# Kernel optimization log

Hardware: AMD Instinct MI355X
Metric: run time of the kernel (lower is better)

Reference implementation:

```python
import jax, jax.numpy as jnp
import numpy as np


def _rotate_half(x):
    a, b = jnp.split(x, 2, axis=-1)
    return jnp.concatenate([-b, a], axis=-1)


def _rope_tables(L, d, dtype):
    inv = 1.0 / (10000.0 ** (jnp.arange(0, d, 2, dtype=jnp.float32) / d))
    ang = jnp.arange(L, dtype=jnp.float32)[:, None] * inv[None, :]  # (L, d/2)
    cos = jnp.repeat(jnp.cos(ang), 2, axis=-1)[None, :, None, :].astype(dtype)  # (1,L,1,d)
    sin = jnp.repeat(jnp.sin(ang), 2, axis=-1)[None, :, None, :].astype(dtype)
    return cos, sin


def setup_inputs() -> dict:
    key = jax.random.key(0)
    ks = jax.random.split(key, 7)
    B, L, D, h = 1, 1024, 768, 12
    d = D // h
    s = 0.02
    return {
        "X": jax.random.normal(ks[0], (B, L, D), jnp.float32),
        "Wq": jax.random.normal(ks[1], (D, D), jnp.float32) * s,
        "Wk": jax.random.normal(ks[2], (D, D), jnp.float32) * s,
        "Wv": jax.random.normal(ks[3], (D, D), jnp.float32) * s,
        "Wu": jax.random.normal(ks[4], (D, D), jnp.float32) * s,
        "Wg": jax.random.normal(ks[5], (3 * h, D), jnp.float32) * s,
        "Wo": jax.random.normal(ks[6], (D, D), jnp.float32) * s,
        "prior_mu": jnp.zeros((1, 1, h, d), jnp.float32),
        "prior_log_tau": jnp.zeros((1, 1, h, 1), jnp.float32),
    }


def _forward(X, Wq, Wk, Wv, Wu, Wg, Wo, prior_mu, prior_log_tau):
    B, L, D = X.shape
    h = prior_mu.shape[2]
    d = D // h
    eps = 1e-12
    # projections (torch Linear: x @ W.T, no bias)
    q = (X @ Wq.T).reshape(B, L, h, d)
    k = (X @ Wk.T).reshape(B, L, h, d)
    v = (X @ Wv.T).reshape(B, L, h, d)
    u = (X @ Wu.T).reshape(B, L, h, d)
    gate = (X @ Wg.T).reshape(B, L, h, 3)
    t = jnp.arange(1, L + 1, dtype=X.dtype).reshape(1, L, 1, 1)
    # calculate_logit (logit_type='deviation', causal)
    log_tau = jnp.exp(jnp.clip(prior_log_tau, -50.0, 30.0))
    u_sum = jnp.cumsum(u, axis=1)
    bar_u = (log_tau * prior_mu + u_sum) / (log_tau + t)
    s_i = -jnp.sum(u * bar_u, axis=-1, keepdims=True) / np.float32(np.sqrt(d))  # (B,L,h,1)
    # RoPE + L2 normalize q, k
    cos, sin = _rope_tables(L, d, X.dtype)
    q = q * cos + _rotate_half(q) * sin
    k = k * cos + _rotate_half(k) * sin
    q = q / jnp.maximum(jnp.linalg.norm(q, axis=-1, keepdims=True), eps)
    k = k / jnp.maximum(jnp.linalg.norm(k, axis=-1, keepdims=True), eps)
    # associative causal branch of compute_o
    s_max = jax.lax.stop_gradient(jnp.max(s_i, axis=1, keepdims=True))
    exp_s = jnp.exp(s_i - s_max)              # (B,L,h,1)
    E_t = jnp.cumsum(exp_s, axis=1)
    P_t = jnp.cumsum(s_i, axis=1)
    kv = jnp.einsum('blhd,blhe->blhde', k, v)  # (B,L,h,d,d)
    F_t = jnp.cumsum(exp_s[..., None] * kv, axis=1)
    G_t = jnp.cumsum(s_i[..., None] * kv, axis=1)
    H_t = jnp.cumsum(kv, axis=1)
    sig1 = jax.nn.sigmoid(gate[..., 0:1])      # (B,L,h,1)
    sigh = jax.nn.sigmoid(gate[..., 1:2])
    alpha = sigh / (E_t + eps)
    beta = (sig1 - sigh) / t
    gamma = -((beta * P_t + sigh) / t)
    M = alpha[..., None] * F_t + beta[..., None] * G_t + gamma[..., None] * H_t
    out = jnp.einsum('blhd,blhde->blhe', q, M)  # (B,L,h,d)
    # LayerNorm over head dim, eps=1e-5, no affine
    mu = jnp.mean(out, axis=-1, keepdims=True)
    var = jnp.mean(jnp.square(out - mu), axis=-1, keepdims=True)
    out = (out - mu) / jnp.sqrt(var + 1e-5)
    # output projection (dropout=0.0 -> identity)
    return out.reshape(B, L, D) @ Wo.T


def reference(X, Wq, Wk, Wv, Wu, Wg, Wo, prior_mu, prior_log_tau):
    return _forward(X, Wq, Wk, Wv, Wu, Wg, Wo, prior_mu, prior_log_tau)
```

## Files before the change

### kernel.cpp

```cpp
#include <hip/hip_runtime.h>
#include <hip/hip_bf16.h>
#include <math.h>

typedef __attribute__((ext_vector_type(8))) short bf16x8;
typedef __attribute__((ext_vector_type(4))) float f32x4;

#define SEQ 1024
#define DIM 768
#define NH 12
#define HD 64


__device__ __forceinline__ float wave_reduce_sum(float v) {
    for (int off = 1; off < 64; off <<= 1) v += __shfl_xor(v, off);
    return v;
}
__device__ __forceinline__ short f2bs(float x) {
    __hip_bfloat16 h = __float2bfloat16(x);
    return *reinterpret_cast<short*>(&h);
}
__device__ __forceinline__ float bs2f(short x) {
    __hip_bfloat16 h = *reinterpret_cast<__hip_bfloat16*>(&x);
    return (float)h;
}
__device__ __forceinline__ bf16x8 cvt8r(const float4& a, const float4& b) {
    bf16x8 r;
    r[0]=f2bs(a.x); r[1]=f2bs(a.y); r[2]=f2bs(a.z); r[3]=f2bs(a.w);
    r[4]=f2bs(b.x); r[5]=f2bs(b.y); r[6]=f2bs(b.z); r[7]=f2bs(b.w);
    return r;
}
__device__ __forceinline__ void async_copy16(const void* gptr, void* ldsbase, int lane) {
#if __has_builtin(__builtin_amdgcn_global_load_lds)
    __builtin_amdgcn_global_load_lds(
        (const __attribute__((address_space(1))) unsigned int*)gptr,
        (__attribute__((address_space(3))) unsigned int*)ldsbase, 16, 0, 0);
#else
    *(bf16x8*)((short*)ldsbase + lane*8) = *(const bf16x8*)gptr;
#endif
}

__global__ __launch_bounds__(256) void k_prep(const float* __restrict__ X,
    const float* __restrict__ Wq, const float* __restrict__ Wk,
    const float* __restrict__ Wv, const float* __restrict__ Wu,
    const float* __restrict__ Wg, const float* __restrict__ Wo,
    short* __restrict__ Xb, short* __restrict__ Wqb, short* __restrict__ Wkb,
    short* __restrict__ Wvb, short* __restrict__ Wub, short* __restrict__ Wgb,
    short* __restrict__ Wob)
{
    int seg = blockIdx.y;
    const float* src; short* dst; int n8;
    switch (seg) {
        case 0: src = X;  dst = Xb;  n8 = 98304; break;
        case 1: src = Wq; dst = Wqb; n8 = 73728; break;
        case 2: src = Wk; dst = Wkb; n8 = 73728; break;
        case 3: src = Wv; dst = Wvb; n8 = 73728; break;
        case 4: src = Wu; dst = Wub; n8 = 73728; break;
        case 5: src = Wg; dst = Wgb; n8 = 3456;  break;
        default: src = Wo; dst = Wob; n8 = 73728; break;
    }
    int i = blockIdx.x*256 + threadIdx.x;
    if (i >= n8) return;
    const float* s = src + (size_t)i*8;
    *(bf16x8*)(dst + (size_t)i*8) = cvt8r(*(const float4*)s, *(const float4*)(s + 4));
}

__global__ __launch_bounds__(256, 4) void k_proj5(const short* __restrict__ Xb,
    const short* __restrict__ Wqb, const short* __restrict__ Wkb,
    const short* __restrict__ Wvb, const short* __restrict__ Wub,
    const short* __restrict__ Wgb,
    __hip_bfloat16* __restrict__ Qb, __hip_bfloat16* __restrict__ Kb,
    __hip_bfloat16* __restrict__ Vt, __hip_bfloat16* __restrict__ Ub,
    float* __restrict__ G)
{
    int t = blockIdx.x;
    int mat, rt, ct;
    if (t < 576)      { int m3 = t/192; mat = (m3==2)?3:m3; int r = t%192; rt = r/12; ct = r%12; }
    else if (t < 768) { mat = 2; int r = t-576; rt = r/16; ct = r%16; }
    else              { mat = 4; rt = t-768; ct = 0; }

    __shared__ short lds[16384];

    int tid = threadIdx.x;
    int wv = tid>>6, lane = tid&63, g = lane>>4, n = lane&15;
    int wm = wv>>1, wn = wv&1;

    const short* Asrc; const short* Bsrc; int arow0, brow0, Brows;
    if (mat == 2) { Asrc = Wvb; Bsrc = Xb; arow0 = rt*64; brow0 = ct*64; Brows = SEQ; }
    else {
        Asrc = Xb; arow0 = rt*64; brow0 = ct*64;
        Bsrc = (mat==0)?Wqb:(mat==1)?Wkb:(mat==3)?Wub:Wgb;
        Brows = (mat==4) ? 36 : DIM;
    }

    auto dma_step = [&](int buf, int k0) {
        short* Ab = lds + buf*4096;
        short* Bb = lds + 8192 + buf*4096;
        for (int p = 0; p < 2; ++p) {
            int sbase = p*256 + wv*64;
            int s = sbase + lane;
            int r = s >> 3, c = s & 7, cl = c ^ (r & 7);
            async_copy16(Asrc + (size_t)(arow0 + r)*DIM + k0 + cl*8, Ab + sbase*8, lane);
            int gr = brow0 + r; if (gr >= Brows) gr = Brows - 1;
            async_copy16(Bsrc + (size_t)gr*DIM + k0 + cl*8, Bb + sbase*8, lane);
        }
    };

    f32x4 acc[2][2];
    for (int i=0;i<2;++i) for (int j=0;j<2;++j) acc[i][j] = (f32x4){0,0,0,0};

    dma_step(0, 0);
    for (int it = 0; it < 12; ++it) {
        __syncthreads();
        if (it < 11) dma_step(1 - (it & 1), (it + 1)*64);
        int buf = it & 1;
        const short* Ab = lds + buf*4096;
        const short* Bb = lds + 8192 + buf*4096;
        for (int ks = 0; ks < 2; ++ks) {
            int q = ks*4 + g;
            bf16x8 af[2], bfr[2];
            for (int i=0;i<2;++i)
                af[i] = *(const bf16x8*)(&Ab[((wm*32+i*16+n)*8 + (q ^ (n&7)))*8]);
            for (int j=0;j<2;++j)
                bfr[j] = *(const bf16x8*)(&Bb[((wn*32+j*16+n)*8 + (q ^ (n&7)))*8]);
            for (int i=0;i<2;++i)
                for (int j=0;j<2;++j)
                    acc[i][j] = __builtin_amdgcn_mfma_f32_16x16x32_bf16(af[i], bfr[j], acc[i][j], 0,0,0);
        }
    }
    __syncthreads();

    if (mat == 4) {
        for (int i=0;i<2;++i) for (int j=0;j<2;++j) for (int r=0;r<4;++r) {
            int row = rt*64 + wm*32 + i*16 + g*4 + r;
            int col = wn*32 + j*16 + n;
            if (col < 36) G[(size_t)row*36 + col] = acc[i][j][r];
        }
        return;
    }

    short* C = lds;
    for (int i=0;i<2;++i) for (int j=0;j<2;++j) for (int r=0;r<4;++r)
        C[(wm*32 + i*16 + g*4 + r)*64 + wn*32 + j*16 + n] = f2bs(acc[i][j][r]);
    __syncthreads();

    if (mat == 2) {
        const unsigned int* Cu = (const unsigned int*)C;
        for (int k = 0; k < 8; ++k) {
            int idx = k*256 + tid;
            int row = idx >> 5, cu = idx & 31;
            ((unsigned int*)(Vt + (size_t)(rt*64 + row)*SEQ + ct*64))[cu] = Cu[row*32 + cu];
        }
    } else if (mat == 3) {
        const unsigned int* Cu = (const unsigned int*)C;
        for (int k = 0; k < 8; ++k) {
            int idx = k*256 + tid;
            int row = idx >> 5, cu = idx & 31;
            ((unsigned int*)(Ub + ((size_t)ct*SEQ + rt*64 + row)*HD))[cu] = Cu[row*32 + cu];
        }
    } else {
        __hip_bfloat16* dst = (mat==0) ? Qb : Kb;
        int i2 = lane >> 1;
        float inv = expf((float)i2 * (-9.210340371976184f / 32.f));
        float c0, s0, C1, S1;
        sincosf((float)(rt*64 + wv*16) * inv, &s0, &c0);
        sincosf(inv, &S1, &C1);
        for (int k = 0; k < 16; ++k) {
            int row = wv*16 + k;
            int l = rt*64 + row;
            float x = bs2f(C[row*64 + lane]);
            float p = __shfl(x, lane ^ 32);
            float rot = (lane < 32) ? -p : p;
            float y = x*c0 + rot*s0;
            float nrm = wave_reduce_sum(y*y);
            y = y / fmaxf(sqrtf(nrm), 1e-12f);
            dst[((size_t)ct*SEQ + l)*HD + lane] = __float2bfloat16(y);
            float cn = c0*C1 - s0*S1;
            s0 = s0*C1 + c0*S1;
            c0 = cn;
        }
    }
}

__global__ __launch_bounds__(256) void k_si(const __hip_bfloat16* __restrict__ Ub,
    const float* __restrict__ pmu, const float* __restrict__ plt,
    float* __restrict__ si_)
{
    int T = blockIdx.x, h = blockIdx.y;
    int wv = threadIdx.x >> 6, lane = threadIdx.x & 63;
    int g = lane >> 4, n = lane & 15;
    int lbase = T*16;
    const short* ub = (const short*)Ub + (size_t)h*SEQ*HD;
    __shared__ float pbuf[4][16];

    bf16x8 a0 = *(const bf16x8*)(ub + (size_t)(lbase + n)*HD + g*8);
    bf16x8 a1 = *(const bf16x8*)(ub + (size_t)(lbase + n)*HD + 32 + g*8);

    float p[4] = {0.f, 0.f, 0.f, 0.f};

    for (int jt = wv; jt < T; jt += 4) {
        const short* br = ub + (size_t)(jt*16 + n)*HD + g*8;
        bf16x8 b0 = *(const bf16x8*)br;
        bf16x8 b1 = *(const bf16x8*)(br + 32);
        f32x4 sacc = {0.f,0.f,0.f,0.f};
        sacc = __builtin_amdgcn_mfma_f32_16x16x32_bf16(a0, b0, sacc, 0,0,0);
        sacc = __builtin_amdgcn_mfma_f32_16x16x32_bf16(a1, b1, sacc, 0,0,0);
        for (int r = 0; r < 4; ++r) p[r] += sacc[r];
    }
    if (wv == 0) {
        const short* br = ub + (size_t)(lbase + n)*HD + g*8;
        bf16x8 b0 = *(const bf16x8*)br;
        bf16x8 b1 = *(const bf16x8*)(br + 32);
        f32x4 d = {0.f,0.f,0.f,0.f};
        d = __builtin_amdgcn_mfma_f32_16x16x32_bf16(a0, b0, d, 0,0,0);
        d = __builtin_amdgcn_mfma_f32_16x16x32_bf16(a1, b1, d, 0,0,0);
        for (int r = 0; r < 4; ++r) if (n <= g*4 + r) p[r] += d[r];
    }
    if (wv == 1) {
        float ltau = expf(fminf(fmaxf(plt[h], -50.f), 30.f));
        for (int r = 0; r < 4; ++r) {
            int l = lbase + g*4 + r;
            float acc = 0.f;
            for (int c = n; c < 64; c += 16)
                acc += bs2f(ub[(size_t)l*HD + c]) * pmu[h*HD + c];
            p[r] += ltau * acc;
        }
    }
    for (int off = 1; off < 16; off <<= 1)
        for (int r = 0; r < 4; ++r) p[r] += __shfl_xor(p[r], off);
    if (n == 0)
        for (int r = 0; r < 4; ++r) pbuf[wv][g*4 + r] = p[r];
    __syncthreads();
    if (wv == 0 && n == 0) {
        float ltau = expf(fminf(fmaxf(plt[h], -50.f), 30.f));
        for (int r = 0; r < 4; ++r) {
            int row = g*4 + r, l = lbase + row;
            float tot = pbuf[0][row] + pbuf[1][row] + pbuf[2][row] + pbuf[3][row];
            si_[h*SEQ + l] = -tot * 0.125f / (ltau + (float)(l + 1));
        }
    }
}

__global__ __launch_bounds__(64) void k_scan2(const float* __restrict__ G,
    const float* __restrict__ si_, float* __restrict__ es_,
    float* __restrict__ al_, float* __restrict__ be_, float* __restrict__ ga_)
{
    int h = blockIdx.x, lane = threadIdx.x;
    const float* si = si_ + h*SEQ;
    int base = lane * 16;
    float sv[16], ev[16];
    float vm = -1e30f;
#pragma unroll
    for (int i = 0; i < 16; ++i) { sv[i] = si[base + i]; vm = fmaxf(vm, sv[i]); }
    for (int off = 1; off < 64; off <<= 1) vm = fmaxf(vm, __shfl_xor(vm, off));
    float se = 0.f, ss = 0.f;
#pragma unroll
    for (int i = 0; i < 16; ++i) {
        ev[i] = expf(fminf(sv[i] - vm, 0.f));
        se += ev[i]; ss += sv[i];
    }
    float pe = se, ps = ss;
    for (int off = 1; off < 64; off <<= 1) {
        float t1 = __shfl_up(pe, off), t2 = __shfl_up(ps, off);
        if (lane >= off) { pe += t1; ps += t2; }
    }
    float E = pe - se, P = ps - ss;
#pragma unroll
    for (int i = 0; i < 16; ++i) {
        int l = base + i;
        E += ev[i]; P += sv[i];
        float t = (float)(l + 1);
        float s1 = 1.f / (1.f + expf(-G[(size_t)l*36 + h*3 + 0]));
        float sh = 1.f / (1.f + expf(-G[(size_t)l*36 + h*3 + 1]));
        float a = sh / (E + 1e-12f);
        float b = (s1 - sh) / t;
        float gm = -((b * P + sh) / t);
        es_[h*SEQ + l] = ev[i];
        al_[h*SEQ + l] = a;
        be_[h*SEQ + l] = b;
        ga_[h*SEQ + l] = gm;
    }
}

__global__ __launch_bounds__(256) void k_attn(const __hip_bfloat16* __restrict__ Qb,
    const __hip_bfloat16* __restrict__ Kb, const __hip_bfloat16* __restrict__ Vt,
    const float* __restrict__ si_, const float* __restrict__ es_,
    const float* __restrict__ al_, const float* __restrict__ be_,
    const float* __restrict__ ga_, __hip_bfloat16* __restrict__ opre)
{
    int t = blockIdx.x, h = blockIdx.y;
    int wv = threadIdx.x >> 6, lane = threadIdx.x & 63;
    int g = lane >> 4, n = lane & 15;
    __shared__ short P[4][16*64];
    __shared__ float Op[4][16][64];
    short* Pw = P[wv];
    int m0 = t*16;
    const short* qrow = (const short*)Qb + ((size_t)h*SEQ + m0 + n)*HD + g*8;
    bf16x8 qa0 = *(const bf16x8*)qrow;
    bf16x8 qa1 = *(const bf16x8*)(qrow + 32);
    const float* al = al_ + h*SEQ;
    const float* be = be_ + h*SEQ;
    const float* ga = ga_ + h*SEQ;
    const float* es = es_ + h*SEQ;
    const float* si = si_ + h*SEQ;
    float A_[4], B_[4], G_[4];
    for (int r = 0; r < 4; ++r) {
        int m = m0 + g*4 + r;
        A_[r] = al[m]; B_[r] = be[m]; G_[r] = ga[m];
    }
    f32x4 acco[4];
    for (int et = 0; et < 4; ++et) acco[et] = (f32x4){0.f,0.f,0.f,0.f};

    int jtmax = t >> 2;
    for (int jt = wv; jt <= jtmax; jt += 4) {
        int j0 = jt*64;
        for (int ct = 0; ct < 4; ++ct) {
            const short* krow = (const short*)Kb + ((size_t)h*SEQ + j0 + ct*16 + n)*HD + g*8;
            bf16x8 kb0 = *(const bf16x8*)krow;
            bf16x8 kb1 = *(const bf16x8*)(krow + 32);
            f32x4 sacc = {0.f,0.f,0.f,0.f};
            sacc = __builtin_amdgcn_mfma_f32_16x16x32_bf16(qa0, kb0, sacc, 0, 0, 0);
            sacc = __builtin_amdgcn_mfma_f32_16x16x32_bf16(qa1, kb1, sacc, 0, 0, 0);
            int j = j0 + ct*16 + n;
            float ej = es[j], sj = si[j];
            int chunk = ct*2 + (n>>3), e = n&7;
            for (int r = 0; r < 4; ++r) {
                int m = m0 + g*4 + r;
                float w = (j <= m) ? (A_[r]*ej + B_[r]*sj + G_[r]) : 0.f;
                int ml = g*4 + r;
                Pw[ml*64 + (chunk ^ (ml&7))*8 + e] = f2bs(w * sacc[r]);
            }
        }
        const short* vb = (const short*)Vt + (size_t)h*HD*SEQ;
        for (int et = 0; et < 4; ++et) {
            for (int sub = 0; sub < 2; ++sub) {
                int q = sub*4 + g;
                bf16x8 pa = *(const bf16x8*)(&Pw[n*64 + (q ^ (n&7))*8]);
                bf16x8 vfr = *(const bf16x8*)(vb + (size_t)(et*16 + n)*SEQ + j0 + sub*32 + g*8);
                acco[et] = __builtin_amdgcn_mfma_f32_16x16x32_bf16(pa, vfr, acco[et], 0, 0, 0);
            }
        }
    }
    for (int et = 0; et < 4; ++et)
        for (int r = 0; r < 4; ++r)
            Op[wv][g*4 + r][et*16 + n] = acco[et][r];
    __syncthreads();
    for (int rr = 0; rr < 4; ++rr) {
        int row = wv*4 + rr;
        float v = Op[0][row][lane] + Op[1][row][lane] + Op[2][row][lane] + Op[3][row][lane];
        float sm = wave_reduce_sum(v);
        float sq = wave_reduce_sum(v*v);
        float mu = sm * (1.f/64.f);
        float var = fmaxf(sq * (1.f/64.f) - mu*mu, 0.f);
        float invs = rsqrtf(var + 1e-5f);
        opre[(size_t)(m0 + row)*DIM + h*HD + lane] = __float2bfloat16((v - mu) * invs);
    }
}

__global__ __launch_bounds__(256, 4) void k_oproj(const short* __restrict__ A,
    const short* __restrict__ Wob, float* __restrict__ out)
{
    int rt = blockIdx.x, ct = blockIdx.y;
    __shared__ short lds[16384];

    int tid = threadIdx.x;
    int wv = tid>>6, lane = tid&63, g = lane>>4, n = lane&15;
    int wm = wv>>1, wn = wv&1;

    auto dma_step = [&](int buf, int k0) {
        short* Ab = lds + buf*4096;
        short* Bb = lds + 8192 + buf*4096;
        for (int p = 0; p < 2; ++p) {
            int sbase = p*256 + wv*64;
            int s = sbase + lane;
            int r = s >> 3, c = s & 7, cl = c ^ (r & 7);
            async_copy16(A + (size_t)(rt*64 + r)*DIM + k0 + cl*8, Ab + sbase*8, lane);
            async_copy16(Wob + (size_t)(ct*64 + r)*DIM + k0 + cl*8, Bb + sbase*8, lane);
        }
    };

    f32x4 acc[2][2];
    for (int i=0;i<2;++i) for (int j=0;j<2;++j) acc[i][j] = (f32x4){0,0,0,0};

    dma_step(0, 0);
    for (int it = 0; it < 12; ++it) {
        __syncthreads();
        if (it < 11) dma_step(1 - (it & 1), (it + 1)*64);
        int buf = it & 1;
        const short* Ab = lds + buf*4096;
        const short* Bb = lds + 8192 + buf*4096;
        for (int ks = 0; ks < 2; ++ks) {
            int q = ks*4 + g;
            bf16x8 af[2], bfr[2];
            for (int i=0;i<2;++i)
                af[i] = *(const bf16x8*)(&Ab[((wm*32+i*16+n)*8 + (q ^ (n&7)))*8]);
            for (int j=0;j<2;++j)
                bfr[j] = *(const bf16x8*)(&Bb[((wn*32+j*16+n)*8 + (q ^ (n&7)))*8]);
            for (int i=0;i<2;++i)
                for (int j=0;j<2;++j)
                    acc[i][j] = __builtin_amdgcn_mfma_f32_16x16x32_bf16(af[i], bfr[j], acc[i][j], 0,0,0);
        }
    }
    for (int i=0;i<2;++i) for (int j=0;j<2;++j) for (int r=0;r<4;++r) {
        int row = rt*64 + wm*32 + i*16 + g*4 + r;
        int col = ct*64 + wn*32 + j*16 + n;
        out[(size_t)row*DIM + col] = acc[i][j][r];
    }
}

extern "C" void kernel_launch(void* const* d_in, const int* in_sizes, int n_in,
                              void* d_out, int out_size, void* d_ws, size_t ws_size,
                              hipStream_t stream) {
    const float* X   = (const float*)d_in[0];
    const float* Wq  = (const float*)d_in[1];
    const float* Wk  = (const float*)d_in[2];
    const float* Wv  = (const float*)d_in[3];
    const float* Wu  = (const float*)d_in[4];
    const float* Wg  = (const float*)d_in[5];
    const float* Wo  = (const float*)d_in[6];
    const float* pmu = (const float*)d_in[7];
    const float* plt = (const float*)d_in[8];

    char* w = (char*)d_ws;
    __hip_bfloat16* Qb   = (__hip_bfloat16*)(w + 0);
    __hip_bfloat16* Kb   = (__hip_bfloat16*)(w + 1572864);
    __hip_bfloat16* Vt   = (__hip_bfloat16*)(w + 3145728);
    __hip_bfloat16* opre = (__hip_bfloat16*)(w + 4718592);
    float*          G    = (float*)(w + 6291456);
    float*          si_  = (float*)(w + 6438912);
    float*          es_  = si_ + NH*SEQ;
    float*          al_  = es_ + NH*SEQ;
    float*          be_  = al_ + NH*SEQ;
    float*          ga_  = be_ + NH*SEQ;
    short*          Xb   = (short*)(w + 6684672);
    short*          Wqb  = (short*)(w + 8257536);
    short*          Wkb  = (short*)(w + 9437184);
    short*          Wvb  = (short*)(w + 10616832);
    short*          Wub  = (short*)(w + 11796480);
    short*          Wgb  = (short*)(w + 12976128);
    short*          Wob  = (short*)(w + 13031424);
    __hip_bfloat16* Ub   = (__hip_bfloat16*)d_out;
    float*          out  = (float*)d_out;

    hipLaunchKernelGGL(k_prep, dim3(384, 7), dim3(256), 0, stream,
                       X, Wq, Wk, Wv, Wu, Wg, Wo, Xb, Wqb, Wkb, Wvb, Wub, Wgb, Wob);
    hipLaunchKernelGGL(k_proj5, dim3(784), dim3(256), 0, stream,
                       Xb, Wqb, Wkb, Wvb, Wub, Wgb, Qb, Kb, Vt, Ub, G);
    hipLaunchKernelGGL(k_si, dim3(64, NH), dim3(256), 0, stream,
                       Ub, pmu, plt, si_);
    hipLaunchKernelGGL(k_scan2, dim3(NH), dim3(64), 0, stream,
                       G, si_, es_, al_, be_, ga_);
    hipLaunchKernelGGL(k_attn, dim3(64, NH), dim3(256), 0, stream,
                       Qb, Kb, Vt, si_, es_, al_, be_, ga_, opre);
    hipLaunchKernelGGL(k_oproj, dim3(16, 12), dim3(256), 0, stream,
                       (const short*)opre, Wob, out);
}
```

Baseline: 149.0 us.

## Fuse softmax-stat scan into attention kernel, recomputing prefix sums per block

Removes the separate k_scan2 kernel. Each attention block now computes its own running max, exp-sum and s-sum over the causal prefix of s_i, then derives the alpha, beta and gamma coefficients for its 16 rows in shared memory. The exp weights are recomputed inline from s_i instead of being loaded. Each block uses the max over its own prefix rather than the global max, which still gives the same alpha·F ratio because the same shift is applied to both. This saves a launch and a low-parallelism serial kernel, in exchange for redundant prefix reductions and extra exp work in every attention block.

New measurement: 144.5 us. -3.0%, faster.

```diff
diff --git a/kernel.cpp b/kernel.cpp
--- a/kernel.cpp
+++ b/kernel.cpp
@@ -240,72 +240,68 @@
     }
 }
 
-__global__ __launch_bounds__(64) void k_scan2(const float* __restrict__ G,
-    const float* __restrict__ si_, float* __restrict__ es_,
-    float* __restrict__ al_, float* __restrict__ be_, float* __restrict__ ga_)
-{
-    int h = blockIdx.x, lane = threadIdx.x;
-    const float* si = si_ + h*SEQ;
-    int base = lane * 16;
-    float sv[16], ev[16];
-    float vm = -1e30f;
-#pragma unroll
-    for (int i = 0; i < 16; ++i) { sv[i] = si[base + i]; vm = fmaxf(vm, sv[i]); }
-    for (int off = 1; off < 64; off <<= 1) vm = fmaxf(vm, __shfl_xor(vm, off));
-    float se = 0.f, ss = 0.f;
-#pragma unroll
-    for (int i = 0; i < 16; ++i) {
-        ev[i] = expf(fminf(sv[i] - vm, 0.f));
-        se += ev[i]; ss += sv[i];
-    }
-    float pe = se, ps = ss;
-    for (int off = 1; off < 64; off <<= 1) {
-        float t1 = __shfl_up(pe, off), t2 = __shfl_up(ps, off);
-        if (lane >= off) { pe += t1; ps += t2; }
-    }
-    float E = pe - se, P = ps - ss;
-#pragma unroll
-    for (int i = 0; i < 16; ++i) {
-        int l = base + i;
-        E += ev[i]; P += sv[i];
-        float t = (float)(l + 1);
-        float s1 = 1.f / (1.f + expf(-G[(size_t)l*36 + h*3 + 0]));
-        float sh = 1.f / (1.f + expf(-G[(size_t)l*36 + h*3 + 1]));
-        float a = sh / (E + 1e-12f);
-        float b = (s1 - sh) / t;
-        float gm = -((b * P + sh) / t);
-        es_[h*SEQ + l] = ev[i];
-        al_[h*SEQ + l] = a;
-        be_[h*SEQ + l] = b;
-        ga_[h*SEQ + l] = gm;
-    }
-}
-
 __global__ __launch_bounds__(256) void k_attn(const __hip_bfloat16* __restrict__ Qb,
     const __hip_bfloat16* __restrict__ Kb, const __hip_bfloat16* __restrict__ Vt,
-    const float* __restrict__ si_, const float* __restrict__ es_,
-    const float* __restrict__ al_, const float* __restrict__ be_,
-    const float* __restrict__ ga_, __hip_bfloat16* __restrict__ opre)
+    const float* __restrict__ si_, const float* __restrict__ Gm,
+    __hip_bfloat16* __restrict__ opre)
 {
     int t = blockIdx.x, h = blockIdx.y;
-    int wv = threadIdx.x >> 6, lane = threadIdx.x & 63;
+    int tid = threadIdx.x;
+    int wv = tid >> 6, lane = tid & 63;
     int g = lane >> 4, n = lane & 15;
     __shared__ short P[4][16*64];
     __shared__ float Op[4][16][64];
+    __shared__ float red[4][2];
+    __shared__ float ABG[3][16];
+    __shared__ float smax_s;
     short* Pw = P[wv];
     int m0 = t*16;
+    const float* si = si_ + h*SEQ;
+
     const short* qrow = (const short*)Qb + ((size_t)h*SEQ + m0 + n)*HD + g*8;
     bf16x8 qa0 = *(const bf16x8*)qrow;
     bf16x8 qa1 = *(const bf16x8*)(qrow + 32);
-    const float* al = al_ + h*SEQ;
-    const float* be = be_ + h*SEQ;
-    const float* ga = ga_ + h*SEQ;
-    const float* es = es_ + h*SEQ;
-    const float* si = si_ + h*SEQ;
+
+    float mx = -1e30f;
+    for (int j = tid; j < m0 + 16; j += 256) mx = fmaxf(mx, si[j]);
+    for (int off = 1; off < 64; off <<= 1) mx = fmaxf(mx, __shfl_xor(mx, off));
+    if (lane == 0) red[wv][0] = mx;
+    __syncthreads();
+    if (tid == 0) smax_s = fmaxf(fmaxf(red[0][0], red[1][0]), fmaxf(red[2][0], red[3][0]));
+    __syncthreads();
+    float sm = smax_s;
+
+    float se = 0.f, ss = 0.f;
+    for (int j = tid; j < m0; j += 256) { float s = si[j]; se += expf(s - sm); ss += s; }
+    se = wave_reduce_sum(se); ss = wave_reduce_sum(ss);
+    __syncthreads();
+    if (lane == 0) { red[wv][0] = se; red[wv][1] = ss; }
+    __syncthreads();
+
+    if (wv == 0 && lane < 16) {
+        float Eb = red[0][0] + red[1][0] + red[2][0] + red[3][0];
+        float Pb = red[0][1] + red[1][1] + red[2][1] + red[3][1];
+        float sv = si[m0 + lane];
+        float pe = expf(sv - sm), ps = sv;
+        for (int off = 1; off < 16; off <<= 1) {
+            float t1 = __shfl_up(pe, off), t2 = __shfl_up(ps, off);
+            if (lane >= off) { pe += t1; ps += t2; }
+        }
+        float E = Eb + pe, Pv = Pb + ps;
+        float tv = (float)(m0 + lane + 1);
+        float s1 = 1.f / (1.f + expf(-Gm[(size_t)(m0 + lane)*36 + h*3 + 0]));
+        float sh = 1.f / (1.f + expf(-Gm[(size_t)(m0 + lane)*36 + h*3 + 1]));
+        float a = sh / (E + 1e-12f);
+        float b = (s1 - sh) / tv;
+        ABG[0][lane] = a;
+        ABG[1][lane] = b;
+        ABG[2][lane] = -((b * Pv + sh) / tv);
+    }
+    __syncthreads();
+
     float A_[4], B_[4], G_[4];
     for (int r = 0; r < 4; ++r) {
-        int m = m0 + g*4 + r;
-        A_[r] = al[m]; B_[r] = be[m]; G_[r] = ga[m];
+        A_[r] = ABG[0][g*4 + r]; B_[r] = ABG[1][g*4 + r]; G_[r] = ABG[2][g*4 + r];
     }
     f32x4 acco[4];
     for (int et = 0; et < 4; ++et) acco[et] = (f32x4){0.f,0.f,0.f,0.f};
@@ -321,7 +317,8 @@
             sacc = __builtin_amdgcn_mfma_f32_16x16x32_bf16(qa0, kb0, sacc, 0, 0, 0);
             sacc = __builtin_amdgcn_mfma_f32_16x16x32_bf16(qa1, kb1, sacc, 0, 0, 0);
             int j = j0 + ct*16 + n;
-            float ej = es[j], sj = si[j];
+            float sj = si[j];
+            float ej = expf(sj - sm);
             int chunk = ct*2 + (n>>3), e = n&7;
             for (int r = 0; r < 4; ++r) {
                 int m = m0 + g*4 + r;
@@ -347,9 +344,9 @@
     for (int rr = 0; rr < 4; ++rr) {
         int row = wv*4 + rr;
         float v = Op[0][row][lane] + Op[1][row][lane] + Op[2][row][lane] + Op[3][row][lane];
-        float sm = wave_reduce_sum(v);
+        float sm2 = wave_reduce_sum(v);
         float sq = wave_reduce_sum(v*v);
-        float mu = sm * (1.f/64.f);
+        float mu = sm2 * (1.f/64.f);
         float var = fmaxf(sq * (1.f/64.f) - mu*mu, 0.f);
         float invs = rsqrtf(var + 1e-5f);
         opre[(size_t)(m0 + row)*DIM + h*HD + lane] = __float2bfloat16((v - mu) * invs);
@@ -427,10 +424,6 @@
     __hip_bfloat16* opre = (__hip_bfloat16*)(w + 4718592);
     float*          G    = (float*)(w + 6291456);
     float*          si_  = (float*)(w + 6438912);
-    float*          es_  = si_ + NH*SEQ;
-    float*          al_  = es_ + NH*SEQ;
-    float*          be_  = al_ + NH*SEQ;
-    float*          ga_  = be_ + NH*SEQ;
     short*          Xb   = (short*)(w + 6684672);
     short*          Wqb  = (short*)(w + 8257536);
     short*          Wkb  = (short*)(w + 9437184);
@@ -447,10 +440,8 @@
                        Xb, Wqb, Wkb, Wvb, Wub, Wgb, Qb, Kb, Vt, Ub, G);
     hipLaunchKernelGGL(k_si, dim3(64, NH), dim3(256), 0, stream,
                        Ub, pmu, plt, si_);
-    hipLaunchKernelGGL(k_scan2, dim3(NH), dim3(64), 0, stream,
-                       G, si_, es_, al_, be_, ga_);
     hipLaunchKernelGGL(k_attn, dim3(64, NH), dim3(256), 0, stream,
-                       Qb, Kb, Vt, si_, es_, al_, be_, ga_, opre);
+                       Qb, Kb, Vt, si_, G, opre);
     hipLaunchKernelGGL(k_oproj, dim3(16, 12), dim3(256), 0, stream,
                        (const short*)opre, Wob, out);
 }
```
